# Performance work log

Hardware: AMD Instinct MI355X
Metric: run time of the kernel (lower is better)

## Reference

```python
import jax, jax.numpy as jnp
import numpy as np

THETA = 10000.0
NUM_HEADS = 16
MAX_SEQ_LEN = 2048

def _rope_tables(d_k, max_seq_len, theta=THETA):
    dims = jnp.arange(0, d_k, 2, dtype=jnp.float32)
    freqs = 1.0 / theta ** (dims / d_k)
    t = jnp.arange(max_seq_len, dtype=jnp.float32)
    angles = jnp.outer(t, freqs)  # (max_seq_len, d_k//2)
    return jnp.cos(angles), jnp.sin(angles)

def _apply_rope(x, token_positions, cos_tab, sin_tab):
    # x: (..., seq_len, d_k)
    cos = jnp.repeat(cos_tab[token_positions], 2, axis=-1)  # (seq_len, d_k)
    sin = jnp.repeat(sin_tab[token_positions], 2, axis=-1)
    # interleaved rotate-half: (-x1, x0, -x3, x2, ...)
    xp = x.reshape(*x.shape[:-1], -1, 2)
    x_neg = jnp.stack([-xp[..., 1], xp[..., 0]], axis=-1).reshape(x.shape)
    return x * cos + x_neg * sin

def setup_inputs() -> dict:
    key = jax.random.key(0)
    ks = jax.random.split(key, 5)
    B, S, D = 4, 2048, 1024
    scale = 1.0 / np.sqrt(D)
    return {
        "x": jax.random.normal(ks[0], (B, S, D), dtype=jnp.float32),
        "q_proj": jax.random.normal(ks[1], (D, D), dtype=jnp.float32) * scale,
        "k_proj": jax.random.normal(ks[2], (D, D), dtype=jnp.float32) * scale,
        "v_proj": jax.random.normal(ks[3], (D, D), dtype=jnp.float32) * scale,
        "o_proj": jax.random.normal(ks[4], (D, D), dtype=jnp.float32) * scale,
        "token_positions": jnp.arange(S, dtype=jnp.int64),
    }

def reference(x, q_proj, k_proj, v_proj, o_proj, token_positions):
    B, S, D = x.shape
    H = NUM_HEADS
    d_k = D // H
    cos_tab, sin_tab = _rope_tables(d_k, MAX_SEQ_LEN)

    q = (x @ q_proj).reshape(B, S, H, d_k).transpose(0, 2, 1, 3)  # (B,H,S,d_k)
    k = (x @ k_proj).reshape(B, S, H, d_k).transpose(0, 2, 1, 3)
    v = (x @ v_proj).reshape(B, S, H, d_k).transpose(0, 2, 1, 3)

    q = _apply_rope(q, token_positions, cos_tab, sin_tab)
    k = _apply_rope(k, token_positions, cos_tab, sin_tab)

    scores = jnp.einsum('bhqd,bhkd->bhqk', q, k) / jnp.sqrt(jnp.float32(d_k))
    causal = jnp.tril(jnp.ones((S, S), dtype=bool))
    scores = jnp.where(causal, scores, -jnp.inf)
    attn = jax.nn.softmax(scores, axis=-1)
    out = jnp.einsum('bhqk,bhkd->bhqd', attn, v)  # (B,H,S,d_k)
    out = out.transpose(0, 2, 1, 3).reshape(B, S, D)
    return out @ o_proj
```

## Files before the change

### kernel.cpp

```cpp
#include <hip/hip_runtime.h>
#include <hip/hip_bf16.h>
#include <stdint.h>


typedef __attribute__((ext_vector_type(8))) short short8;
typedef __attribute__((ext_vector_type(4))) float floatx4;
typedef __attribute__((ext_vector_type(16))) float floatx16;

#define MFMA16(a,b,c) __builtin_amdgcn_mfma_f32_16x16x32_bf16((a),(b),(c),0,0,0)
#define MFMA32(a,b,c) __builtin_amdgcn_mfma_f32_32x32x16_bf16((a),(b),(c),0,0,0)
#define BAR() __builtin_amdgcn_s_barrier()
#define LGKM0 asm volatile("s_waitcnt lgkmcnt(0)" ::: "memory")
#define VMCNT6 asm volatile("s_waitcnt vmcnt(6)" ::: "memory")

__device__ __forceinline__ uint32_t fbits(float f){ uint32_t u; __builtin_memcpy(&u,&f,4); return u; }
__device__ __forceinline__ unsigned short f2bf(float f) {
    uint32_t u = fbits(f);
    return (unsigned short)((u + 0x7fffu + ((u>>16)&1u)) >> 16);
}
__device__ __forceinline__ float bf2f(unsigned short s){ uint32_t u = (uint32_t)s<<16; float f; __builtin_memcpy(&f,&u,4); return f; }
__device__ __forceinline__ uint32_t pkbf(float lo, float hi) {
#if __has_builtin(__builtin_amdgcn_cvt_pk_bf16_f32)
    auto r = __builtin_amdgcn_cvt_pk_bf16_f32(lo, hi);
    uint32_t u; __builtin_memcpy(&u, &r, sizeof(u));
    return u;
#else
    return __builtin_amdgcn_perm(fbits(hi)+0x8000u, fbits(lo)+0x8000u, 0x07060302u);
#endif
}
__device__ __forceinline__ float fexp2(float x) {
#if __has_builtin(__builtin_amdgcn_exp2f)
    return __builtin_amdgcn_exp2f(x);
#else
    return exp2f(x);
#endif
}

__device__ __forceinline__ void load_lds16(const unsigned short* g, unsigned short* l) {
    __builtin_amdgcn_global_load_lds(
        (const __attribute__((address_space(1))) void*)g,
        (__attribute__((address_space(3))) void*)l, 16, 0, 0);
}

__device__ __forceinline__ bool sniff_f32(const unsigned short* xr) {
    int lane = threadIdx.x & 63;
    int bad = 0;
#pragma unroll
    for (int i = 0; i < 16; i++) {
        float v = bf2f(xr[lane * 16 + i]);
        if (!(__builtin_fabsf(v) < 1e10f)) bad = 1;
    }
    return __ballot(bad != 0) != 0ull;
}

__global__ __launch_bounds__(256) void prep_k(
    const void* __restrict__ x,
    const void* __restrict__ wq, const void* __restrict__ wk,
    const void* __restrict__ wv, const void* __restrict__ wo,
    unsigned short* __restrict__ WT, unsigned short* __restrict__ WoT,
    float2* __restrict__ tab, unsigned short* __restrict__ xb) {
    int blk = blockIdx.x, t = threadIdx.x;
    bool f32 = sniff_f32((const unsigned short*)x);
    if (blk < 4096) {
        __shared__ unsigned short tile[32][33];
        int mat = blk >> 10, r = blk & 1023;
        const void* src = (mat == 0) ? wq : (mat == 1) ? wk : (mat == 2) ? wv : wo;
        unsigned short* dst = (mat < 3) ? (WT + (size_t)mat * 1048576) : WoT;
        int bx = (r & 31) * 32, by = (r >> 5) * 32;
        int tx = t & 31, ty = t >> 5;
#pragma unroll
        for (int j = 0; j < 32; j += 8) {
            size_t idx = (size_t)(by + ty + j) * 1024 + bx + tx;
            float v = f32 ? ((const float*)src)[idx] : bf2f(((const unsigned short*)src)[idx]);
            tile[ty + j][tx] = f2bf(v);
        }
        __syncthreads();
#pragma unroll
        for (int j = 0; j < 32; j += 8)
            dst[(size_t)(bx + ty + j) * 1024 + by + tx] = tile[tx][ty + j];
    } else if (blk < 4352) {
        int i = (blk - 4096) * 256 + t;
        int pos = i >> 5, j = i & 31;
        float freq = exp2f(-(float)(2 * j) * (1.0f / 64.0f) * 13.287712379549449f);
        float a = (float)pos * freq;
        tab[i] = make_float2(cosf(a), sinf(a));
    } else {
        size_t base = (size_t)(blk - 4352) * 2048 + (size_t)t * 8;
        if (f32) {
            const float4* s4 = (const float4*)((const float*)x + base);
            float4 a = s4[0], b = s4[1];
            uint4 o;
            o.x = pkbf(a.x, a.y); o.y = pkbf(a.z, a.w);
            o.z = pkbf(b.x, b.y); o.w = pkbf(b.z, b.w);
            *(uint4*)(xb + base) = o;
        } else {
            *(uint4*)(xb + base) = *(const uint4*)((const unsigned short*)x + base);
        }
    }
}

template <int MODE>
__global__ __launch_bounds__(512, 2) void gemm8(
    const unsigned short* __restrict__ A,
    const unsigned short* __restrict__ Bt,
    void* __restrict__ C0,
    unsigned short* __restrict__ C1,
    unsigned short* __restrict__ C2,
    const float2* __restrict__ tab,
    const unsigned short* __restrict__ xsniff) {
    const int K = 1024;
    extern __shared__ __align__(16) char smraw[];
    unsigned short* Asm = (unsigned short*)smraw;
    unsigned short* Bsm = Asm + 3 * 8192;

    int t = threadIdx.x;
    int lane = t & 63, w = t >> 6;
    int quad = lane >> 4, l15 = lane & 15;
    int wm = (w >> 2) * 64, wn = (w & 3) * 64;

    int nbx = gridDim.x;
    int flat = blockIdx.y * nbx + blockIdx.x;
    int cpx = (nbx * gridDim.y) >> 3;
    int swzid = (flat & 7) * cpx + (flat >> 3);
    int bx = swzid % nbx, by = swzid / nbx;
    int m0 = by * 128, n0 = bx * 256;

    floatx4 acc[4][4];
#pragma unroll
    for (int i = 0; i < 4; i++)
#pragma unroll
        for (int j = 0; j < 4; j++) acc[i][j] = (floatx4){0.f, 0.f, 0.f, 0.f};

    int srow = t >> 3;
    int sg = ((t & 7) ^ (srow & 7)) * 8;
    const unsigned short* gA = A + (size_t)(m0 + srow) * K + sg;
    const unsigned short* gB = Bt + (size_t)(n0 + srow) * K + sg;
    unsigned short* lA = Asm + w * 512;
    unsigned short* lB = Bsm + w * 512;

    int rA[4], rB[4], ce[2];
#pragma unroll
    for (int m = 0; m < 4; m++) rA[m] = (wm + m * 16 + l15) * 64;
#pragma unroll
    for (int n = 0; n < 4; n++) rB[n] = (wn + n * 16 + l15) * 64;
#pragma unroll
    for (int ks = 0; ks < 2; ks++)
        ce[ks] = ((ks * 64 + quad * 16) ^ ((l15 & 7) << 4)) >> 1;

#pragma unroll
    for (int kt = 0; kt < 2; kt++) {
#pragma unroll
        for (int h = 0; h < 2; h++)
            load_lds16(gA + (size_t)h * 64 * K + kt * 64, lA + kt * 8192 + h * 4096);
#pragma unroll
        for (int c = 0; c < 4; c++)
            load_lds16(gB + (size_t)c * 64 * K + kt * 64, lB + kt * 16384 + c * 4096);
    }
    VMCNT6;
    __syncthreads();

    int cur = 0, nxt = 2;
#pragma unroll 1
    for (int kt = 0; kt < 16; kt++) {
        const unsigned short* cA = Asm + cur * 8192;
        const unsigned short* cB = Bsm + cur * 16384;
        unsigned short* nA = lA + nxt * 8192;
        unsigned short* nB = lB + nxt * 16384;
        size_t ko = (size_t)(kt + 2) * 64;
        short8 a0[4], a1[4], bf0, bf1;

#pragma unroll
        for (int m = 0; m < 4; m++) a0[m] = *(const short8*)(cA + rA[m] + ce[0]);
        bf0 = *(const short8*)(cB + rB[0] + ce[0]);
        bf1 = *(const short8*)(cB + rB[1] + ce[0]);
        load_lds16(gA + ko, nA);
        load_lds16(gA + (size_t)64 * K + ko, nA + 4096);
        BAR(); LGKM0;
        __builtin_amdgcn_s_setprio(1);
#pragma unroll
        for (int m = 0; m < 4; m++) {
            acc[m][0] = MFMA16(a0[m], bf0, acc[m][0]);
            acc[m][1] = MFMA16(a0[m], bf1, acc[m][1]);
        }
        __builtin_amdgcn_s_setprio(0);
        BAR();

        bf0 = *(const short8*)(cB + rB[2] + ce[0]);
        bf1 = *(const short8*)(cB + rB[3] + ce[0]);
        load_lds16(gB + ko, nB);
        load_lds16(gB + (size_t)64 * K + ko, nB + 4096);
        BAR(); LGKM0;
        __builtin_amdgcn_s_setprio(1);
#pragma unroll
        for (int m = 0; m < 4; m++) {
            acc[m][2] = MFMA16(a0[m], bf0, acc[m][2]);
            acc[m][3] = MFMA16(a0[m], bf1, acc[m][3]);
        }
        __builtin_amdgcn_s_setprio(0);
        BAR();

#pragma unroll
        for (int m = 0; m < 4; m++) a1[m] = *(const short8*)(cA + rA[m] + ce[1]);
        bf0 = *(const short8*)(cB + rB[0] + ce[1]);
        bf1 = *(const short8*)(cB + rB[1] + ce[1]);
        load_lds16(gB + (size_t)128 * K + ko, nB + 8192);
        load_lds16(gB + (size_t)192 * K + ko, nB + 12288);
        BAR(); LGKM0;
        __builtin_amdgcn_s_setprio(1);
#pragma unroll
        for (int m = 0; m < 4; m++) {
            acc[m][0] = MFMA16(a1[m], bf0, acc[m][0]);
            acc[m][1] = MFMA16(a1[m], bf1, acc[m][1]);
        }
        __builtin_amdgcn_s_setprio(0);
        BAR();

        bf0 = *(const short8*)(cB + rB[2] + ce[1]);
        bf1 = *(const short8*)(cB + rB[3] + ce[1]);
        BAR(); LGKM0;
        __builtin_amdgcn_s_setprio(1);
#pragma unroll
        for (int m = 0; m < 4; m++) {
            acc[m][2] = MFMA16(a1[m], bf0, acc[m][2]);
            acc[m][3] = MFMA16(a1[m], bf1, acc[m][3]);
        }
        __builtin_amdgcn_s_setprio(0);
        VMCNT6;
        BAR();

        cur = (cur == 2) ? 0 : cur + 1;
        nxt = (nxt == 2) ? 0 : nxt + 1;
    }

    bool out_f32 = (MODE == 0) ? sniff_f32(xsniff) : false;
#pragma unroll
    for (int i = 0; i < 4; i++) {
#pragma unroll
        for (int j = 0; j < 4; j++) {
            int col = n0 + wn + j * 16 + l15;
            int row0 = m0 + wm + i * 16 + quad * 4;
            if (MODE == 0) {
#pragma unroll
                for (int r = 0; r < 4; r++) {
                    size_t idx = (size_t)(row0 + r) * 1024 + col;
                    if (out_f32) ((float*)C0)[idx] = acc[i][j][r];
                    else ((unsigned short*)C0)[idx] = f2bf(acc[i][j][r]);
                }
            } else {
                int which = col >> 10, nn = col & 1023;
                int b = row0 >> 11, s0 = row0 & 2047;
                if (which == 2) {
                    int hh = nn >> 6, d = nn & 63;
                    uint32_t lo = pkbf(acc[i][j][0], acc[i][j][1]);
                    uint32_t hi = pkbf(acc[i][j][2], acc[i][j][3]);
                    *(uint64_t*)(C2 + ((size_t)((b * 16 + hh) * 64 + d)) * 2048 + s0) =
                        (uint64_t)lo | ((uint64_t)hi << 32);
                } else {
                    int d = nn & 63;
                    unsigned short* dst = (which == 0) ? (unsigned short*)C0 : C1;
                    float sc = (which == 0) ? 0.18033688011112042f : 1.0f;
#pragma unroll
                    for (int r = 0; r < 4; r++) {
                        int s = s0 + r;
                        float v = acc[i][j][r];
                        float pv = __shfl_xor(v, 1);
                        float2 cs = tab[(s << 5) + (d >> 1)];
                        float o = (d & 1) ? (v * cs.x + pv * cs.y) : (v * cs.x - pv * cs.y);
                        dst[((size_t)(b * 2048 + s)) * 1024 + nn] = f2bf(o * sc);
                    }
                }
            }
        }
    }
}

__global__ __launch_bounds__(512, 4) void flash_k(
    const unsigned short* __restrict__ Qb,
    const unsigned short* __restrict__ Kb,
    const unsigned short* __restrict__ Vt,
    unsigned short* __restrict__ A2) {
    __shared__ __align__(16) char sm[33792];
    unsigned short* Kl = (unsigned short*)sm;
    unsigned short* Vl = (unsigned short*)(sm + 16384);
    float4* Osw = (float4*)sm;
    float*  lsw = (float*)(sm + 32768);

    int bh = blockIdx.x;
    int y = blockIdx.y;
    int qt = (y < 8) ? (15 - y) : (y - 8);
    int b = bh >> 4, h = bh & 15;
    int t = threadIdx.x, lane = t & 63, w = t >> 6;
    int wq = w & 3, wg = w >> 2;
    int l31 = lane & 31, half = lane >> 5;
    size_t base = ((size_t)b * 2048) * 1024 + h * 64;
    int q0w = qt * 128 + wq * 32;

    short8 Qf[4];
#pragma unroll
    for (int ks = 0; ks < 4; ks++)
        Qf[ks] = *(const short8*)(Qb + base + (size_t)(q0w + l31) * 1024 + ks * 16 + half * 8);

    floatx16 O[2];
    O[0] = (floatx16)0.0f; O[1] = (floatx16)0.0f;
    float lsum = 0.f;

    int nk = 2 * (qt + 1);

    int srow = t >> 3, gs = t & 7;
    const unsigned short* kg = Kb + base + (size_t)srow * 1024 + gs * 8;
    const unsigned short* vg = Vt + ((size_t)(bh * 64 + srow)) * 2048 + gs * 8;
    int sw = srow * 64 + ((gs ^ (srow & 7)) * 8);

    short8 rk = *(const short8*)(kg);
    short8 rv = *(const short8*)(vg);

    for (int kt = 0; kt < nk; kt++) {
        int k0 = kt * 64, bf = kt & 1;
        *(short8*)&Kl[bf * 4096 + sw] = rk;
        *(short8*)&Vl[bf * 4096 + sw] = rv;
        __syncthreads();
        if (kt + 1 < nk) {
            size_t ko = (size_t)(kt + 1) * 64;
            rk = *(const short8*)(kg + ko * 1024);
            rv = *(const short8*)(vg + ko);
        }
        int k0mb = k0 + wg * 32;
        if (k0mb < q0w + 32) {
            const unsigned short* Klb = Kl + bf * 4096;
            const unsigned short* Vlb = Vl + bf * 4096;
            short8 Ka[4];
#pragma unroll
            for (int ks = 0; ks < 4; ks++)
                Ka[ks] = *(const short8*)&Klb[(wg * 32 + l31) * 64 +
                                              (((ks * 2 + half) ^ (l31 & 7)) * 8)];
            floatx16 Sc = (floatx16)0.0f;
#pragma unroll
            for (int ks = 0; ks < 4; ks++)
                Sc = MFMA32(Ka[ks], Qf[ks], Sc);

            bool domask = (k0mb + 31 > q0w);
            int thr = q0w + l31 - k0mb - half * 4;
            float p[16];
#pragma unroll
            for (int e = 0; e < 16; e++) {
                float v = fexp2(Sc[e]);
                if (domask) {
                    const int ce = (e & 3) + ((e >> 2) << 3);
                    v = (ce > thr) ? 0.f : v;
                }
                p[e] = v;
            }
            float t0 = (p[0] + p[1]) + (p[2] + p[3]);
            float t1 = (p[4] + p[5]) + (p[6] + p[7]);
            float t2 = (p[8] + p[9]) + (p[10] + p[11]);
            float t3 = (p[12] + p[13]) + (p[14] + p[15]);
            lsum += (t0 + t1) + (t2 + t3);
            uint32_t pkm[8];
#pragma unroll
            for (int jj = 0; jj < 8; jj++)
                pkm[jj] = pkbf(p[2 * jj], p[2 * jj + 1]);

            short8 Va[2][2];
#pragma unroll
            for (int db = 0; db < 2; db++)
#pragma unroll
                for (int ks2 = 0; ks2 < 2; ks2++)
                    Va[db][ks2] = *(const short8*)&Vlb[(db * 32 + l31) * 64 +
                                                       ((((wg * 2 + ks2) * 2 + half) ^ (l31 & 7)) * 8)];
#pragma unroll
            for (int ks2 = 0; ks2 < 2; ks2++) {
                uint32_t p0 = pkm[4 * ks2 + 0];
                uint32_t p1 = pkm[4 * ks2 + 1];
                uint32_t p2 = pkm[4 * ks2 + 2];
                uint32_t p3 = pkm[4 * ks2 + 3];
                uint32_t u = half ? p0 : p2;
                uint32_t v2 = half ? p1 : p3;
                uint32_t ya = (uint32_t)__shfl_xor((int)u, 32);
                uint32_t yb = (uint32_t)__shfl_xor((int)v2, 32);
                union { short8 s; uint32_t q[4]; } bb;
                bb.q[0] = half ? ya : p0;
                bb.q[1] = half ? yb : p1;
                bb.q[2] = half ? p2 : ya;
                bb.q[3] = half ? p3 : yb;
#pragma unroll
                for (int db = 0; db < 2; db++)
                    O[db] = MFMA32(Va[db][ks2], bb.s, O[db]);
            }
        }
    }

    __syncthreads();
    if (w < 4) {
#pragma unroll
        for (int db = 0; db < 2; db++)
#pragma unroll
            for (int g = 0; g < 4; g++)
                Osw[(w * 8 + db * 4 + g) * 64 + lane] =
                    make_float4(O[db][g * 4 + 0], O[db][g * 4 + 1],
                                O[db][g * 4 + 2], O[db][g * 4 + 3]);
        lsw[w * 64 + lane] = lsum;
    }
    __syncthreads();
    if (w >= 4) {
        int wp = w - 4;
#pragma unroll
        for (int db = 0; db < 2; db++)
#pragma unroll
            for (int g = 0; g < 4; g++) {
                float4 o = Osw[(wp * 8 + db * 4 + g) * 64 + lane];
                O[db][g * 4 + 0] += o.x;
                O[db][g * 4 + 1] += o.y;
                O[db][g * 4 + 2] += o.z;
                O[db][g * 4 + 3] += o.w;
            }
        lsum += lsw[wp * 64 + lane];
        float tot = lsum + __shfl_xor(lsum, 32);
        float inv = 1.0f / tot;
        int scol = q0w + l31;
        unsigned short* op = A2 + base + (size_t)scol * 1024;
#pragma unroll
        for (int db = 0; db < 2; db++) {
#pragma unroll
            for (int g = 0; g < 4; g++) {
                int d0 = db * 32 + half * 4 + g * 8;
                float v0 = O[db][g * 4 + 0] * inv;
                float v1 = O[db][g * 4 + 1] * inv;
                float v2 = O[db][g * 4 + 2] * inv;
                float v3 = O[db][g * 4 + 3] * inv;
                uint32_t lo = pkbf(v0, v1), hi = pkbf(v2, v3);
                *(uint64_t*)(op + d0) = (uint64_t)lo | ((uint64_t)hi << 32);
            }
        }
    }
}

extern "C" void kernel_launch(void* const* d_in, const int* in_sizes, int n_in,
                              void* d_out, int out_size, void* d_ws, size_t ws_size,
                              hipStream_t stream) {
    const void* x  = d_in[0];
    const void* wq = d_in[1];
    const void* wk = d_in[2];
    const void* wv = d_in[3];
    const void* wo = d_in[4];

    char* ws = (char*)d_ws;
    unsigned short* WT  = (unsigned short*)(ws);
    unsigned short* WoT = (unsigned short*)(ws + 6291456);
    float2*         tab = (float2*)(ws + 8388608);
    unsigned short* xb  = (unsigned short*)(ws + 8913920);
    unsigned short* Qb  = (unsigned short*)(ws + 8913920 + 16777216ull);
    unsigned short* Kb  = (unsigned short*)(ws + 8913920 + 2ull * 16777216);
    unsigned short* Vt  = (unsigned short*)(ws + 8913920 + 3ull * 16777216);
    unsigned short* A2  = xb;

    (void)hipFuncSetAttribute(reinterpret_cast<const void*>(gemm8<1>),
                              hipFuncAttributeMaxDynamicSharedMemorySize, 147456);
    (void)hipFuncSetAttribute(reinterpret_cast<const void*>(gemm8<0>),
                              hipFuncAttributeMaxDynamicSharedMemorySize, 147456);

    prep_k<<<8448, 256, 0, stream>>>(x, wq, wk, wv, wo, WT, WoT, tab, xb);

    gemm8<1><<<dim3(12, 64), 512, 147456, stream>>>(xb, WT, Qb, Kb, Vt, tab,
                                                    (const unsigned short*)x);
    flash_k<<<dim3(64, 16), 512, 0, stream>>>(Qb, Kb, Vt, A2);
    gemm8<0><<<dim3(4, 64), 512, 147456, stream>>>(A2, WoT, d_out, nullptr, nullptr, tab,
                                                   (const unsigned short*)x);
}
```

Baseline: 252.4 us.

## Replace QKV projection GEMM with 256x256-tile kernel using 16x16 MFMA

Adds a new QKV projection kernel that computes 256x256 output tiles (each wave owns 128x64) with a K-step of 32, triple-buffered LDS and loads interleaved between two MFMA phases. The epilogue still applies RoPE, the Q scale and the V transpose. Larger tiles raise arithmetic intensity and halve the grid to 384 blocks. In exchange each thread holds more accumulator registers and the grid is smaller, which may cost occupancy or leave compute units less evenly loaded.

```diff
diff --git a/kernel.cpp b/kernel.cpp
--- a/kernel.cpp
+++ b/kernel.cpp
@@ -11,6 +11,7 @@
 #define MFMA32(a,b,c) __builtin_amdgcn_mfma_f32_32x32x16_bf16((a),(b),(c),0,0,0)
 #define BAR() __builtin_amdgcn_s_barrier()
 #define LGKM0 asm volatile("s_waitcnt lgkmcnt(0)" ::: "memory")
+#define VMCNT4 asm volatile("s_waitcnt vmcnt(4)" ::: "memory")
 #define VMCNT6 asm volatile("s_waitcnt vmcnt(6)" ::: "memory")
 
 __device__ __forceinline__ uint32_t fbits(float f){ uint32_t u; __builtin_memcpy(&u,&f,4); return u; }
@@ -99,6 +100,128 @@
     }
 }
 
+__global__ __launch_bounds__(512, 2) void gemm32(
+    const unsigned short* __restrict__ A,
+    const unsigned short* __restrict__ Bt,
+    unsigned short* __restrict__ C0,
+    unsigned short* __restrict__ C1,
+    unsigned short* __restrict__ C2,
+    const float2* __restrict__ tab) {
+    const int K = 1024;
+    extern __shared__ __align__(16) char smraw[];
+    unsigned short* SL = (unsigned short*)smraw;
+
+    int t = threadIdx.x;
+    int lane = t & 63, w = t >> 6;
+    int quad = lane >> 4, l15 = lane & 15;
+    int wm = (w >> 2) * 128, wn = (w & 3) * 64;
+
+    int flat = blockIdx.y * 12 + blockIdx.x;
+    int swzid = (flat & 7) * 48 + (flat >> 3);
+    int bx = swzid % 12, by = swzid / 12;
+    int m0 = by * 256, n0 = bx * 256;
+
+    floatx4 acc[8][4];
+#pragma unroll
+    for (int i = 0; i < 8; i++)
+#pragma unroll
+        for (int j = 0; j < 4; j++) acc[i][j] = (floatx4){0.f, 0.f, 0.f, 0.f};
+
+    int srow = t >> 2;
+    int sg = ((t & 3) ^ ((t >> 3) & 3)) * 8;
+    const unsigned short* gA = A + (size_t)(m0 + srow) * K + sg;
+    const unsigned short* gB = Bt + (size_t)(n0 + srow) * K + sg;
+
+    int colsw = (quad ^ ((l15 >> 1) & 3)) * 8;
+    int rAo = (wm + l15) * 32 + colsw;
+    int rBo = 8192 + (wn + l15) * 32 + colsw;
+
+#pragma unroll
+    for (int kt = 0; kt < 2; kt++) {
+        unsigned short* Sb = SL + kt * 16384 + w * 512;
+        load_lds16(gA + kt * 32, Sb);
+        load_lds16(gA + (size_t)128 * K + kt * 32, Sb + 4096);
+        load_lds16(gB + kt * 32, Sb + 8192);
+        load_lds16(gB + (size_t)128 * K + kt * 32, Sb + 12288);
+    }
+    VMCNT4;
+    __syncthreads();
+
+    int cur = 0, nxt = 2;
+#pragma unroll 1
+    for (int kt = 0; kt < 32; kt++) {
+        const unsigned short* cA = SL + cur * 16384 + rAo;
+        const unsigned short* cB = SL + cur * 16384 + rBo;
+        unsigned short* Sb = SL + nxt * 16384 + w * 512;
+        int kc = (kt < 30) ? (kt + 2) : 31;
+        size_t ko = (size_t)kc * 32;
+        short8 af[4], bf[4];
+
+#pragma unroll
+        for (int m = 0; m < 4; m++) af[m] = *(const short8*)(cA + m * 512);
+#pragma unroll
+        for (int j = 0; j < 4; j++) bf[j] = *(const short8*)(cB + j * 512);
+        load_lds16(gA + ko, Sb);
+        load_lds16(gA + (size_t)128 * K + ko, Sb + 4096);
+        BAR(); LGKM0;
+        __builtin_amdgcn_s_setprio(1);
+#pragma unroll
+        for (int m = 0; m < 4; m++)
+#pragma unroll
+            for (int j = 0; j < 4; j++) acc[m][j] = MFMA16(af[m], bf[j], acc[m][j]);
+        __builtin_amdgcn_s_setprio(0);
+        BAR();
+
+#pragma unroll
+        for (int m = 0; m < 4; m++) af[m] = *(const short8*)(cA + (m + 4) * 512);
+        load_lds16(gB + ko, Sb + 8192);
+        load_lds16(gB + (size_t)128 * K + ko, Sb + 12288);
+        BAR(); LGKM0;
+        __builtin_amdgcn_s_setprio(1);
+#pragma unroll
+        for (int m = 0; m < 4; m++)
+#pragma unroll
+            for (int j = 0; j < 4; j++) acc[m + 4][j] = MFMA16(af[m], bf[j], acc[m + 4][j]);
+        __builtin_amdgcn_s_setprio(0);
+        VMCNT4;
+        BAR();
+
+        cur = (cur == 2) ? 0 : cur + 1;
+        nxt = (nxt == 2) ? 0 : nxt + 1;
+    }
+
+#pragma unroll
+    for (int i = 0; i < 8; i++) {
+#pragma unroll
+        for (int j = 0; j < 4; j++) {
+            int col = n0 + wn + j * 16 + l15;
+            int row0 = m0 + wm + i * 16 + quad * 4;
+            int which = col >> 10, nn = col & 1023;
+            int b = row0 >> 11, s0 = row0 & 2047;
+            if (which == 2) {
+                int hh = nn >> 6, d = nn & 63;
+                uint32_t lo = pkbf(acc[i][j][0], acc[i][j][1]);
+                uint32_t hi = pkbf(acc[i][j][2], acc[i][j][3]);
+                *(uint64_t*)(C2 + ((size_t)((b * 16 + hh) * 64 + d)) * 2048 + s0) =
+                    (uint64_t)lo | ((uint64_t)hi << 32);
+            } else {
+                int d = nn & 63;
+                unsigned short* dst = (which == 0) ? C0 : C1;
+                float sc = (which == 0) ? 0.18033688011112042f : 1.0f;
+#pragma unroll
+                for (int r = 0; r < 4; r++) {
+                    int s = s0 + r;
+                    float v = acc[i][j][r];
+                    float pv = __shfl_xor(v, 1);
+                    float2 cs = tab[(s << 5) + (d >> 1)];
+                    float o = (d & 1) ? (v * cs.x + pv * cs.y) : (v * cs.x - pv * cs.y);
+                    dst[((size_t)(b * 2048 + s)) * 1024 + nn] = f2bf(o * sc);
+                }
+            }
+        }
+    }
+}
+
 template <int MODE>
 __global__ __launch_bounds__(512, 2) void gemm8(
     const unsigned short* __restrict__ A,
@@ -453,15 +576,14 @@
     unsigned short* Vt  = (unsigned short*)(ws + 8913920 + 3ull * 16777216);
     unsigned short* A2  = xb;
 
-    (void)hipFuncSetAttribute(reinterpret_cast<const void*>(gemm8<1>),
-                              hipFuncAttributeMaxDynamicSharedMemorySize, 147456);
+    (void)hipFuncSetAttribute(reinterpret_cast<const void*>(gemm32),
+                              hipFuncAttributeMaxDynamicSharedMemorySize, 98304);
     (void)hipFuncSetAttribute(reinterpret_cast<const void*>(gemm8<0>),
                               hipFuncAttributeMaxDynamicSharedMemorySize, 147456);
 
     prep_k<<<8448, 256, 0, stream>>>(x, wq, wk, wv, wo, WT, WoT, tab, xb);
 
-    gemm8<1><<<dim3(12, 64), 512, 147456, stream>>>(xb, WT, Qb, Kb, Vt, tab,
-                                                    (const unsigned short*)x);
+    gemm32<<<dim3(12, 32), 512, 98304, stream>>>(xb, WT, Qb, Kb, Vt, tab);
     flash_k<<<dim3(64, 16), 512, 0, stream>>>(Qb, Kb, Vt, A2);
     gemm8<0><<<dim3(4, 64), 512, 147456, stream>>>(A2, WoT, d_out, nullptr, nullptr, tab,
                                                    (const unsigned short*)x);
```

Result: slower. 263.7 us (+4.5%).

## Restructure GEMM to 4 waves with 128x64 warp tiles and K=32 stages

Applied to the files above, without the earlier changes.

The projection GEMMs drop from 8 to 4 waves per block, and each wave now computes a 128x64 output tile with 32 accumulators. The K step shrinks from 64 to 32, doubling the main-loop iteration count. The four barrier-separated sub-phases per iteration collapse into a single load-then-MFMA phase, and the LDS footprint is halved with a new swizzle. This aims to cut barrier and LDS-read overhead per MFMA through larger per-wave register reuse, at the cost of higher register pressure and fewer waves to hide latency.

```diff
diff --git a/kernel.cpp b/kernel.cpp
--- a/kernel.cpp
+++ b/kernel.cpp
@@ -10,7 +10,6 @@
 #define MFMA16(a,b,c) __builtin_amdgcn_mfma_f32_16x16x32_bf16((a),(b),(c),0,0,0)
 #define MFMA32(a,b,c) __builtin_amdgcn_mfma_f32_32x32x16_bf16((a),(b),(c),0,0,0)
 #define BAR() __builtin_amdgcn_s_barrier()
-#define LGKM0 asm volatile("s_waitcnt lgkmcnt(0)" ::: "memory")
 #define VMCNT6 asm volatile("s_waitcnt vmcnt(6)" ::: "memory")
 
 __device__ __forceinline__ uint32_t fbits(float f){ uint32_t u; __builtin_memcpy(&u,&f,4); return u; }
@@ -100,7 +99,7 @@
 }
 
 template <int MODE>
-__global__ __launch_bounds__(512, 2) void gemm8(
+__global__ __launch_bounds__(256, 2) void gemmp(
     const unsigned short* __restrict__ A,
     const unsigned short* __restrict__ Bt,
     void* __restrict__ C0,
@@ -110,13 +109,12 @@
     const unsigned short* __restrict__ xsniff) {
     const int K = 1024;
     extern __shared__ __align__(16) char smraw[];
-    unsigned short* Asm = (unsigned short*)smraw;
-    unsigned short* Bsm = Asm + 3 * 8192;
+    unsigned short* SL = (unsigned short*)smraw;
 
     int t = threadIdx.x;
     int lane = t & 63, w = t >> 6;
     int quad = lane >> 4, l15 = lane & 15;
-    int wm = (w >> 2) * 64, wn = (w & 3) * 64;
+    int wn = w * 64;
 
     int nbx = gridDim.x;
     int flat = blockIdx.y * nbx + blockIdx.x;
@@ -125,106 +123,66 @@
     int bx = swzid % nbx, by = swzid / nbx;
     int m0 = by * 128, n0 = bx * 256;
 
-    floatx4 acc[4][4];
-#pragma unroll
-    for (int i = 0; i < 4; i++)
+    floatx4 acc[8][4];
+#pragma unroll
+    for (int i = 0; i < 8; i++)
 #pragma unroll
         for (int j = 0; j < 4; j++) acc[i][j] = (floatx4){0.f, 0.f, 0.f, 0.f};
 
-    int srow = t >> 3;
-    int sg = ((t & 7) ^ (srow & 7)) * 8;
-    const unsigned short* gA = A + (size_t)(m0 + srow) * K + sg;
-    const unsigned short* gB = Bt + (size_t)(n0 + srow) * K + sg;
-    unsigned short* lA = Asm + w * 512;
-    unsigned short* lB = Bsm + w * 512;
-
-    int rA[4], rB[4], ce[2];
-#pragma unroll
-    for (int m = 0; m < 4; m++) rA[m] = (wm + m * 16 + l15) * 64;
-#pragma unroll
-    for (int n = 0; n < 4; n++) rB[n] = (wn + n * 16 + l15) * 64;
-#pragma unroll
-    for (int ks = 0; ks < 2; ks++)
-        ce[ks] = ((ks * 64 + quad * 16) ^ ((l15 & 7) << 4)) >> 1;
+    int sg = ((t & 3) ^ ((t >> 3) & 3)) * 8;
+    const unsigned short* gA = A + (size_t)(m0 + (t >> 2)) * K + sg;
+    const unsigned short* gB = Bt + (size_t)(n0 + (t >> 2)) * K + sg;
+
+    int colsw = (quad ^ ((l15 >> 1) & 3)) * 8;
 
 #pragma unroll
     for (int kt = 0; kt < 2; kt++) {
-#pragma unroll
-        for (int h = 0; h < 2; h++)
-            load_lds16(gA + (size_t)h * 64 * K + kt * 64, lA + kt * 8192 + h * 4096);
-#pragma unroll
-        for (int c = 0; c < 4; c++)
-            load_lds16(gB + (size_t)c * 64 * K + kt * 64, lB + kt * 16384 + c * 4096);
+        unsigned short* Sb = SL + kt * 12288 + w * 512;
+        load_lds16(gA + kt * 32, Sb);
+        load_lds16(gA + (size_t)64 * K + kt * 32, Sb + 2048);
+        load_lds16(gB + kt * 32, Sb + 4096);
+        load_lds16(gB + (size_t)64 * K + kt * 32, Sb + 6144);
+        load_lds16(gB + (size_t)128 * K + kt * 32, Sb + 8192);
+        load_lds16(gB + (size_t)192 * K + kt * 32, Sb + 10240);
     }
     VMCNT6;
     __syncthreads();
 
     int cur = 0, nxt = 2;
 #pragma unroll 1
-    for (int kt = 0; kt < 16; kt++) {
-        const unsigned short* cA = Asm + cur * 8192;
-        const unsigned short* cB = Bsm + cur * 16384;
-        unsigned short* nA = lA + nxt * 8192;
-        unsigned short* nB = lB + nxt * 16384;
-        size_t ko = (size_t)(kt + 2) * 64;
-        short8 a0[4], a1[4], bf0, bf1;
-
-#pragma unroll
-        for (int m = 0; m < 4; m++) a0[m] = *(const short8*)(cA + rA[m] + ce[0]);
-        bf0 = *(const short8*)(cB + rB[0] + ce[0]);
-        bf1 = *(const short8*)(cB + rB[1] + ce[0]);
-        load_lds16(gA + ko, nA);
-        load_lds16(gA + (size_t)64 * K + ko, nA + 4096);
-        BAR(); LGKM0;
+    for (int kt = 0; kt < 32; kt++) {
+        const unsigned short* cA = SL + cur * 12288;
+        const unsigned short* cB = SL + cur * 12288 + 4096;
+        unsigned short* Sb = SL + nxt * 12288 + w * 512;
+        int kc = (kt < 30) ? (kt + 2) : 31;
+        size_t ko = (size_t)kc * 32;
+        short8 af[8], bf[4];
+
+#pragma unroll
+        for (int n = 0; n < 4; n++)
+            bf[n] = *(const short8*)(cB + (wn + n * 16 + l15) * 32 + colsw);
+#pragma unroll
+        for (int m = 0; m < 8; m++)
+            af[m] = *(const short8*)(cA + (m * 16 + l15) * 32 + colsw);
+
+        load_lds16(gA + ko, Sb);
+        load_lds16(gA + (size_t)64 * K + ko, Sb + 2048);
+        load_lds16(gB + ko, Sb + 4096);
+        load_lds16(gB + (size_t)64 * K + ko, Sb + 6144);
+        load_lds16(gB + (size_t)128 * K + ko, Sb + 8192);
+        load_lds16(gB + (size_t)192 * K + ko, Sb + 10240);
+
         __builtin_amdgcn_s_setprio(1);
 #pragma unroll
-        for (int m = 0; m < 4; m++) {
-            acc[m][0] = MFMA16(a0[m], bf0, acc[m][0]);
-            acc[m][1] = MFMA16(a0[m], bf1, acc[m][1]);
-        }
+        for (int m = 0; m < 4; m++)
+#pragma unroll
+            for (int n = 0; n < 4; n++) acc[m][n] = MFMA16(af[m], bf[n], acc[m][n]);
+#pragma unroll
+        for (int m = 4; m < 8; m++)
+#pragma unroll
+            for (int n = 0; n < 4; n++) acc[m][n] = MFMA16(af[m], bf[n], acc[m][n]);
         __builtin_amdgcn_s_setprio(0);
-        BAR();
-
-        bf0 = *(const short8*)(cB + rB[2] + ce[0]);
-        bf1 = *(const short8*)(cB + rB[3] + ce[0]);
-        load_lds16(gB + ko, nB);
-        load_lds16(gB + (size_t)64 * K + ko, nB + 4096);
-        BAR(); LGKM0;
-        __builtin_amdgcn_s_setprio(1);
-#pragma unroll
-        for (int m = 0; m < 4; m++) {
-            acc[m][2] = MFMA16(a0[m], bf0, acc[m][2]);
-            acc[m][3] = MFMA16(a0[m], bf1, acc[m][3]);
-        }
-        __builtin_amdgcn_s_setprio(0);
-        BAR();
-
-#pragma unroll
-        for (int m = 0; m < 4; m++) a1[m] = *(const short8*)(cA + rA[m] + ce[1]);
-        bf0 = *(const short8*)(cB + rB[0] + ce[1]);
-        bf1 = *(const short8*)(cB + rB[1] + ce[1]);
-        load_lds16(gB + (size_t)128 * K + ko, nB + 8192);
-        load_lds16(gB + (size_t)192 * K + ko, nB + 12288);
-        BAR(); LGKM0;
-        __builtin_amdgcn_s_setprio(1);
-#pragma unroll
-        for (int m = 0; m < 4; m++) {
-            acc[m][0] = MFMA16(a1[m], bf0, acc[m][0]);
-            acc[m][1] = MFMA16(a1[m], bf1, acc[m][1]);
-        }
-        __builtin_amdgcn_s_setprio(0);
-        BAR();
-
-        bf0 = *(const short8*)(cB + rB[2] + ce[1]);
-        bf1 = *(const short8*)(cB + rB[3] + ce[1]);
-        BAR(); LGKM0;
-        __builtin_amdgcn_s_setprio(1);
-#pragma unroll
-        for (int m = 0; m < 4; m++) {
-            acc[m][2] = MFMA16(a1[m], bf0, acc[m][2]);
-            acc[m][3] = MFMA16(a1[m], bf1, acc[m][3]);
-        }
-        __builtin_amdgcn_s_setprio(0);
+
         VMCNT6;
         BAR();
 
@@ -234,11 +192,11 @@
 
     bool out_f32 = (MODE == 0) ? sniff_f32(xsniff) : false;
 #pragma unroll
-    for (int i = 0; i < 4; i++) {
+    for (int i = 0; i < 8; i++) {
 #pragma unroll
         for (int j = 0; j < 4; j++) {
             int col = n0 + wn + j * 16 + l15;
-            int row0 = m0 + wm + i * 16 + quad * 4;
+            int row0 = m0 + i * 16 + quad * 4;
             if (MODE == 0) {
 #pragma unroll
                 for (int r = 0; r < 4; r++) {
@@ -453,16 +411,16 @@
     unsigned short* Vt  = (unsigned short*)(ws + 8913920 + 3ull * 16777216);
     unsigned short* A2  = xb;
 
-    (void)hipFuncSetAttribute(reinterpret_cast<const void*>(gemm8<1>),
-                              hipFuncAttributeMaxDynamicSharedMemorySize, 147456);
-    (void)hipFuncSetAttribute(reinterpret_cast<const void*>(gemm8<0>),
-                              hipFuncAttributeMaxDynamicSharedMemorySize, 147456);
+    (void)hipFuncSetAttribute(reinterpret_cast<const void*>(gemmp<1>),
+                              hipFuncAttributeMaxDynamicSharedMemorySize, 73728);
+    (void)hipFuncSetAttribute(reinterpret_cast<const void*>(gemmp<0>),
+                              hipFuncAttributeMaxDynamicSharedMemorySize, 73728);
 
     prep_k<<<8448, 256, 0, stream>>>(x, wq, wk, wv, wo, WT, WoT, tab, xb);
 
-    gemm8<1><<<dim3(12, 64), 512, 147456, stream>>>(xb, WT, Qb, Kb, Vt, tab,
-                                                    (const unsigned short*)x);
+    gemmp<1><<<dim3(12, 64), 256, 73728, stream>>>(xb, WT, Qb, Kb, Vt, tab,
+                                                   (const unsigned short*)x);
     flash_k<<<dim3(64, 16), 512, 0, stream>>>(Qb, Kb, Vt, A2);
-    gemm8<0><<<dim3(4, 64), 512, 147456, stream>>>(A2, WoT, d_out, nullptr, nullptr, tab,
-                                                   (const unsigned short*)x);
-}
+    gemmp<0><<<dim3(4, 64), 256, 73728, stream>>>(A2, WoT, d_out, nullptr, nullptr, tab,
+                                                  (const unsigned short*)x);
+}
```

Result: slower. 258.8 us (+2.5%).
